# Optimization experiments

Measured on AMD Instinct MI355X. Metric: run time of the kernel, lower is better.

## Reference

```python
import jax, jax.numpy as jnp
import numpy as np

N_NODES = 200000
N_EDGES = 3200000
N_GRAPHS = 1024
NUM_FEATURES = 8


def _glorot(key, shape):
    fan_in, fan_out = shape
    limit = np.sqrt(6.0 / (fan_in + fan_out))
    return jax.random.uniform(key, shape, jnp.float32, -limit, limit)


def setup_inputs() -> dict:
    key = jax.random.key(0)
    ks = jax.random.split(key, 12)
    x = jax.random.normal(ks[0], (N_NODES, NUM_FEATURES), jnp.float32)
    edge_index = jax.random.randint(ks[1], (2, N_EDGES), 0, N_NODES, jnp.int64)
    batch_index = jnp.sort(jax.random.randint(ks[2], (N_NODES,), 0, N_GRAPHS, jnp.int64))
    params = {
        'W0': _glorot(ks[3], (NUM_FEATURES, 64)), 'b0': jnp.zeros((64,), jnp.float32),
        'W1': _glorot(ks[4], (64, 64)),          'b1': jnp.zeros((64,), jnp.float32),
        'W2': _glorot(ks[5], (64, 32)),          'b2': jnp.zeros((32,), jnp.float32),
        'W3': _glorot(ks[6], (32, 32)),          'b3': jnp.zeros((32,), jnp.float32),
        'Wout': _glorot(ks[7], (64, 10)),        'bout': jnp.zeros((10,), jnp.float32),
    }
    return {'x': x, 'edge_index': edge_index, 'batch_index': batch_index, **params}


def _gcn_conv(x, W, b, src, dst, n_nodes):
    """PyG GCNConv: add self-loops, symmetric deg^-1/2 normalization, x@W, scatter-add, +bias."""
    h = x @ W  # [N, out]
    loops = jnp.arange(n_nodes, dtype=src.dtype)
    s = jnp.concatenate([src, loops])
    d = jnp.concatenate([dst, loops])
    ones = jnp.ones_like(d, dtype=h.dtype)
    deg = jax.ops.segment_sum(ones, d, num_segments=n_nodes)  # in-degree incl. self-loop
    dinv = jnp.where(deg > 0, jax.lax.rsqrt(deg), 0.0)
    norm = dinv[s] * dinv[d]  # [E+N]
    msg = h[s] * norm[:, None]  # gather + scale
    agg = jax.ops.segment_sum(msg, d, num_segments=n_nodes)  # scatter-add at target
    return agg + b


def reference(x, edge_index, batch_index, W0, b0, W1, b1, W2, b2, W3, b3, Wout, bout):
    src, dst = edge_index[0], edge_index[1]
    n = x.shape[0]
    h = jnp.tanh(_gcn_conv(x, W0, b0, src, dst, n))
    h = jax.nn.relu(_gcn_conv(h, W1, b1, src, dst, n))
    h = jax.nn.relu(_gcn_conv(h, W2, b2, src, dst, n))
    h = jax.nn.relu(_gcn_conv(h, W3, b3, src, dst, n))
    # global max pool + global mean pool over graphs in the batch
    gmax = jax.ops.segment_max(h, batch_index, num_segments=N_GRAPHS)
    gsum = jax.ops.segment_sum(h, batch_index, num_segments=N_GRAPHS)
    cnt = jax.ops.segment_sum(jnp.ones((n,), h.dtype), batch_index, num_segments=N_GRAPHS)
    gmean = gsum / jnp.maximum(cnt, 1.0)[:, None]
    pooled = jnp.concatenate([gmax, gmean], axis=1)  # [G, 64]
    return pooled @ Wout + bout  # [G, 10]
```

## Files before the change

### kernel.cpp

```cpp
#include <hip/hip_runtime.h>
#include <hip/hip_fp16.h>

#define TPB 256
#define NB_PART 512
#define NB_LOOP 2048

union H8 { float4 f4; __half2 h2[4]; };
union U2H4 { uint2 u2; __half2 h2[2]; };

__device__ inline void acc_h8(const float4& raw, float* a) {
    H8 u; u.f4 = raw;
#pragma unroll
    for (int i = 0; i < 4; i++) {
        float2 f = __half22float2(u.h2[i]);
        a[2 * i] += f.x;
        a[2 * i + 1] += f.y;
    }
}

__device__ inline void acc_h8x2(const float4& rA, const float4& rB, float* a) {
    H8 uA, uB; uA.f4 = rA; uB.f4 = rB;
#pragma unroll
    for (int i = 0; i < 4; i++) {
        float2 fA = __half22float2(uA.h2[i]);
        float2 fB = __half22float2(uB.h2[i]);
        a[2 * i] += fA.x + fB.x;
        a[2 * i + 1] += fA.y + fB.y;
    }
}

__device__ inline void acc_h8p(const float4& rA, const float4& rB, float* a) {
    H8 uA, uB; uA.f4 = rA; uB.f4 = rB;
#pragma unroll
    for (int i = 0; i < 4; i++) {
        __half2 s = __hadd2(uA.h2[i], uB.h2[i]);
        float2 f = __half22float2(s);
        a[2 * i] += f.x;
        a[2 * i + 1] += f.y;
    }
}

__global__ __launch_bounds__(TPB) void k_bhist(const int* __restrict__ dst,
                                               int* __restrict__ bhist, int E, int shift) {
    __shared__ int h[256];
    int tid = threadIdx.x;
    for (int i = tid; i < 256; i += TPB) h[i] = 0;
    __syncthreads();
    int stride = gridDim.x * TPB;
    for (int e = blockIdx.x * TPB + tid; e < E; e += stride)
        atomicAdd(&h[dst[e] >> shift], 1);
    __syncthreads();
    for (int i = tid; i < 256; i += TPB)
        if (h[i]) atomicAdd(&bhist[i], h[i]);
}

__global__ void k_bscan(const int* __restrict__ bhist, int* __restrict__ bstart,
                        int* __restrict__ gcursor, int nbuck) {
    __shared__ int s[256];
    int tid = threadIdx.x;
    int v = bhist[tid];
    s[tid] = v;
    __syncthreads();
    for (int off = 1; off < 256; off <<= 1) {
        int t = (tid >= off) ? s[tid - off] : 0;
        __syncthreads();
        s[tid] += t;
        __syncthreads();
    }
    int excl = s[tid] - v;
    bstart[tid] = excl;
    if (tid == 255) bstart[256] = s[255];
    if (tid < nbuck) gcursor[tid] = excl;
}

__global__ __launch_bounds__(TPB) void k_part(const int* __restrict__ src,
                                              const int* __restrict__ dst,
                                              int* __restrict__ gcursor,
                                              unsigned* __restrict__ staging,
                                              int E, int shift) {
    __shared__ int hist[256];
    __shared__ int base[256];
    int tid = threadIdx.x;
    long long per = (E + gridDim.x - 1) / gridDim.x;
    int e0 = (int)((long long)blockIdx.x * per);
    int e1 = (int)min((long long)E, (long long)e0 + per);
    for (int i = tid; i < 256; i += TPB) hist[i] = 0;
    __syncthreads();
    for (int e = e0 + tid; e < e1; e += TPB) {
        int b = dst[e] >> shift;
        atomicAdd(&hist[b], 1);
    }
    __syncthreads();
    for (int i = tid; i < 256; i += TPB) {
        int c = hist[i];
        base[i] = (c > 0) ? atomicAdd(&gcursor[i], c) : 0;
        hist[i] = 0;
    }
    __syncthreads();
    unsigned lmask = (1u << shift) - 1u;
    for (int e = e0 + tid; e < e1; e += TPB) {
        int d = dst[e];
        int b = d >> shift;
        int p = base[b] + atomicAdd(&hist[b], 1);
        staging[p] = (((unsigned)d & lmask) << 18) | (unsigned)src[e];
    }
}

__global__ __launch_bounds__(TPB) void k_deg_bucket(const unsigned* __restrict__ staging,
                                                    const int* __restrict__ bstart,
                                                    int* __restrict__ deg,
                                                    float* __restrict__ dinv,
                                                    int N, int shift) {
    __shared__ int cnt[4096];
    int b = blockIdx.x;
    int tid = threadIdx.x;
    int base = b << shift;
    int nn = min(1 << shift, N - base);
    for (int i = tid; i < nn; i += TPB) cnt[i] = 0;
    __syncthreads();
    int rs = bstart[b], re = bstart[b + 1];
    for (int j = rs + tid; j < re; j += TPB) atomicAdd(&cnt[staging[j] >> 18], 1);
    __syncthreads();
    for (int i = tid; i < nn; i += TPB) {
        int c = cnt[i];
        deg[base + i] = c;
        dinv[base + i] = rsqrtf((float)c + 1.0f);
    }
}

__global__ __launch_bounds__(TPB) void k_scan1(const int* __restrict__ deg,
                                               int* __restrict__ row_start,
                                               int* __restrict__ bsum, int N) {
    __shared__ int s[TPB];
    int tid = threadIdx.x;
    int i = blockIdx.x * TPB + tid;
    int v = (i < N) ? deg[i] : 0;
    s[tid] = v;
    __syncthreads();
    for (int off = 1; off < TPB; off <<= 1) {
        int t = (tid >= off) ? s[tid - off] : 0;
        __syncthreads();
        s[tid] += t;
        __syncthreads();
    }
    if (i < N) row_start[i] = s[tid] - v;
    if (tid == TPB - 1) bsum[blockIdx.x] = s[tid];
}

__global__ void k_scan2(int* __restrict__ bsum, int nb) {
    __shared__ int s[1024];
    int tid = threadIdx.x;
    int v = (tid < nb) ? bsum[tid] : 0;
    s[tid] = v;
    __syncthreads();
    for (int off = 1; off < 1024; off <<= 1) {
        int t = (tid >= off) ? s[tid - off] : 0;
        __syncthreads();
        s[tid] += t;
        __syncthreads();
    }
    if (tid < nb) bsum[tid] = s[tid] - v;
}

__global__ __launch_bounds__(TPB) void k_scan3(int* __restrict__ row_start,
                                               const int* __restrict__ bsum, int N) {
    int i = blockIdx.x * TPB + threadIdx.x;
    if (i < N) row_start[i] += bsum[blockIdx.x];
}

__global__ __launch_bounds__(TPB) void k_scatter2(const unsigned* __restrict__ staging,
                                                  const int* __restrict__ row_start,
                                                  int* __restrict__ csr,
                                                  int N, int E, int shift) {
    __shared__ int curs[4096];
    int b = blockIdx.x;
    int tid = threadIdx.x;
    int base = b << shift;
    int nn = min(1 << shift, N - base);
    for (int i = tid; i < nn; i += TPB) curs[i] = row_start[base + i];
    __syncthreads();
    int rs = row_start[base];
    int re = (base + nn < N) ? row_start[base + nn] : E;
    for (int j = rs + tid; j < re; j += TPB) {
        unsigned rec = staging[j];
        int s = rec & 0x3FFFF;
        int dl = rec >> 18;
        int p = atomicAdd(&curs[dl], 1);
        csr[p] = s;
    }
}

__global__ __launch_bounds__(TPB) void k_xp16(const float* __restrict__ x,
                                              const float* __restrict__ dinv,
                                              __half* __restrict__ xp, int N) {
    int t = blockIdx.x * TPB + threadIdx.x;
    if (t < N * 8) xp[t] = __float2half(dinv[t >> 3] * x[t]);
}

__global__ __launch_bounds__(TPB) void k_l0fused(const int* __restrict__ row_start,
                                                 const int* __restrict__ deg,
                                                 const int* __restrict__ csr,
                                                 const float* __restrict__ dinv,
                                                 const __half* __restrict__ xp,
                                                 const float* __restrict__ W0,
                                                 const float* __restrict__ b0,
                                                 __half* __restrict__ h0p, int N) {
    int t = blockIdx.x * TPB + threadIdx.x;
    int node = t >> 4;
    int ll = t & 15;
    if (node >= N) return;
    int s0 = row_start[node], dn = deg[node];
    const float4* x4 = (const float4*)xp;
    float a[8] = {0, 0, 0, 0, 0, 0, 0, 0};
    for (int j = ll; j < dn; j += 16) acc_h8(x4[csr[s0 + j]], a);
#pragma unroll
    for (int off = 1; off < 16; off <<= 1) {
#pragma unroll
        for (int i = 0; i < 8; i++) a[i] += __shfl_xor(a[i], off, 64);
    }
    float di = dinv[node];
    H8 u; u.f4 = x4[node];
    float row[8];
#pragma unroll
    for (int i = 0; i < 4; i++) {
        float2 f = __half22float2(u.h2[i]);
        row[2 * i] = di * (a[2 * i] + f.x);
        row[2 * i + 1] = di * (a[2 * i + 1] + f.y);
    }
    float o[4];
#pragma unroll
    for (int c = 0; c < 4; c++) {
        int f = ll * 4 + c;
        float acc = b0[f];
#pragma unroll
        for (int k = 0; k < 8; k++) acc += row[k] * W0[k * 64 + f];
        o[c] = di * tanhf(acc);
    }
    U2H4 w;
    w.h2[0] = __floats2half2_rn(o[0], o[1]);
    w.h2[1] = __floats2half2_rn(o[2], o[3]);
    ((uint2*)h0p)[(size_t)node * 16 + ll] = w.u2;
}

__global__ __launch_bounds__(TPB) void k_pullmm64h(const int* __restrict__ row_start,
                                                   const int* __restrict__ deg,
                                                   const int* __restrict__ csr,
                                                   const float* __restrict__ dinv,
                                                   const __half* __restrict__ h0p,
                                                   const float* __restrict__ W1,
                                                   const float* __restrict__ b1,
                                                   float* __restrict__ h1, int N) {
    __shared__ float Ws[64 * 64];
    __shared__ float rows[4][64];
    int tid = threadIdx.x;
    for (int i = tid; i < 64 * 64; i += TPB) Ws[i] = W1[i];
    __syncthreads();
    int grp = tid >> 6, lane = tid & 63;
    int q = lane & 7, eg = lane >> 3;
    const float4* h4 = (const float4*)h0p;
    int n4 = (N + 3) >> 2;
    for (int blk = blockIdx.x; blk < n4; blk += gridDim.x) {
        int node = blk * 4 + grp;
        if (node < N) {
            int s0 = row_start[node], dn = deg[node];
            float a[8] = {0, 0, 0, 0, 0, 0, 0, 0};
            int j = eg;
            for (; j + 8 < dn; j += 16) {
                int sA = csr[s0 + j];
                int sB = csr[s0 + j + 8];
                float4 vA = h4[(size_t)sA * 8 + q];
                float4 vB = h4[(size_t)sB * 8 + q];
                acc_h8p(vA, vB, a);
            }
            if (j < dn) acc_h8(h4[(size_t)csr[s0 + j] * 8 + q], a);
#pragma unroll
            for (int off = 8; off < 64; off <<= 1) {
#pragma unroll
                for (int i = 0; i < 8; i++) a[i] += __shfl_xor(a[i], off, 64);
            }
            if (eg == 0) {
                float di = dinv[node];
                H8 u; u.f4 = h4[(size_t)node * 8 + q];
#pragma unroll
                for (int i = 0; i < 4; i++) {
                    float2 f = __half22float2(u.h2[i]);
                    rows[grp][q * 8 + 2 * i] = di * (a[2 * i] + f.x);
                    rows[grp][q * 8 + 2 * i + 1] = di * (a[2 * i + 1] + f.y);
                }
            }
            float acc = b1[lane];
#pragma unroll 8
            for (int k = 0; k < 64; k++) acc += rows[grp][k] * Ws[k * 64 + lane];
            h1[(size_t)node * 64 + lane] = fmaxf(acc, 0.0f);
        }
    }
}

__global__ __launch_bounds__(TPB) void k_mmdh(const float* __restrict__ h,
                                              const float* __restrict__ dinv,
                                              const float* __restrict__ W,
                                              __half* __restrict__ out, int N) {
    __shared__ float Ws[64 * 32];
    __shared__ float rows[4][128];
    int tid = threadIdx.x;
    for (int i = tid; i < 64 * 32; i += TPB) Ws[i] = W[i];
    __syncthreads();
    int grp = tid >> 6, lane = tid & 63;
    int which = lane >> 5, f = lane & 31;
    int n8 = (N + 7) >> 3;
    for (int blk = blockIdx.x; blk < n8; blk += gridDim.x) {
        int nbase = blk * 8 + grp * 2;
        if (nbase < N) rows[grp][lane] = h[(size_t)nbase * 64 + lane];
        if (nbase + 1 < N) rows[grp][64 + lane] = h[(size_t)(nbase + 1) * 64 + lane];
        int n = nbase + which;
        if (n < N) {
            float a = 0.0f;
#pragma unroll 8
            for (int k = 0; k < 64; k++) a += rows[grp][which * 64 + k] * Ws[k * 32 + f];
            out[(size_t)n * 32 + f] = __float2half(dinv[n] * a);
        }
    }
}

__global__ __launch_bounds__(TPB) void k_pullfinmm32h(const int* __restrict__ row_start,
                                                      const int* __restrict__ deg,
                                                      const int* __restrict__ csr,
                                                      const float* __restrict__ dinv,
                                                      const __half* __restrict__ t2p,
                                                      const float* __restrict__ b2,
                                                      const float* __restrict__ W3,
                                                      __half* __restrict__ t3p, int N) {
    __shared__ float Ws[32 * 32];
    __shared__ float rows[4][2][32];
    int tid = threadIdx.x;
    for (int i = tid; i < 32 * 32; i += TPB) Ws[i] = W3[i];
    __syncthreads();
    int grp = tid >> 6, lane = tid & 63;
    int hw = lane >> 5, ll = lane & 31;
    int q = ll & 3, eg = ll >> 2;
    const float4* h4 = (const float4*)t2p;
    int n8 = (N + 7) >> 3;
    for (int blk = blockIdx.x; blk < n8; blk += gridDim.x) {
        int node = blk * 8 + grp * 2 + hw;
        if (node < N) {
            float di = dinv[node];
            int s0 = row_start[node], dn = deg[node];
            float a[8] = {0, 0, 0, 0, 0, 0, 0, 0};
            int j = eg;
            for (; j + 8 < dn; j += 16) {
                int sA = csr[s0 + j];
                int sB = csr[s0 + j + 8];
                float4 vA = h4[(size_t)sA * 4 + q];
                float4 vB = h4[(size_t)sB * 4 + q];
                acc_h8x2(vA, vB, a);
            }
            if (j < dn) acc_h8(h4[(size_t)csr[s0 + j] * 4 + q], a);
#pragma unroll
            for (int off = 4; off < 32; off <<= 1) {
#pragma unroll
                for (int i = 0; i < 8; i++) a[i] += __shfl_xor(a[i], off, 64);
            }
            if (eg == 0) {
                H8 u; u.f4 = h4[(size_t)node * 4 + q];
#pragma unroll
                for (int i = 0; i < 4; i++) {
                    float2 f = __half22float2(u.h2[i]);
                    rows[grp][hw][q * 8 + 2 * i] =
                        fmaxf(di * (a[2 * i] + f.x) + b2[q * 8 + 2 * i], 0.0f);
                    rows[grp][hw][q * 8 + 2 * i + 1] =
                        fmaxf(di * (a[2 * i + 1] + f.y) + b2[q * 8 + 2 * i + 1], 0.0f);
                }
            }
            float a2 = 0.0f;
#pragma unroll 8
            for (int k = 0; k < 32; k++) a2 += rows[grp][hw][k] * Ws[k * 32 + ll];
            t3p[(size_t)node * 32 + ll] = __float2half(di * a2);
        }
    }
}

__global__ __launch_bounds__(TPB) void k_pullfin3h(const int* __restrict__ row_start,
                                                   const int* __restrict__ deg,
                                                   const int* __restrict__ csr,
                                                   const float* __restrict__ dinv,
                                                   const __half* __restrict__ t3p,
                                                   const float* __restrict__ b3,
                                                   float* __restrict__ h3, int N) {
    int t = blockIdx.x * TPB + threadIdx.x;
    int node = t >> 5;
    int ll = t & 31;
    if (node >= N) return;
    int q = ll & 3, eg = ll >> 2;
    int s0 = row_start[node], dn = deg[node];
    const float4* h4 = (const float4*)t3p;
    float a[8] = {0, 0, 0, 0, 0, 0, 0, 0};
    int j = eg;
    for (; j + 8 < dn; j += 16) {
        int sA = csr[s0 + j];
        int sB = csr[s0 + j + 8];
        float4 vA = h4[(size_t)sA * 4 + q];
        float4 vB = h4[(size_t)sB * 4 + q];
        acc_h8x2(vA, vB, a);
    }
    if (j < dn) acc_h8(h4[(size_t)csr[s0 + j] * 4 + q], a);
#pragma unroll
    for (int off = 4; off < 32; off <<= 1) {
#pragma unroll
        for (int i = 0; i < 8; i++) a[i] += __shfl_xor(a[i], off, 64);
    }
    if (eg == 0) {
        float di = dinv[node];
        H8 u; u.f4 = h4[(size_t)node * 4 + q];
        float r[8];
#pragma unroll
        for (int i = 0; i < 4; i++) {
            float2 f = __half22float2(u.h2[i]);
            r[2 * i] = fmaxf(di * (a[2 * i] + f.x) + b3[q * 8 + 2 * i], 0.0f);
            r[2 * i + 1] = fmaxf(di * (a[2 * i + 1] + f.y) + b3[q * 8 + 2 * i + 1], 0.0f);
        }
        float4* o = (float4*)h3 + (size_t)node * 8 + q * 2;
        o[0] = make_float4(r[0], r[1], r[2], r[3]);
        o[1] = make_float4(r[4], r[5], r[6], r[7]);
    }
}

__global__ __launch_bounds__(TPB) void k_gbound(const int* __restrict__ batch,
                                                int* __restrict__ start, int N, int G) {
    int g = blockIdx.x * TPB + threadIdx.x;
    if (g > G) return;
    int lo = 0, hi = N;
    while (lo < hi) {
        int mid = (lo + hi) >> 1;
        if (batch[mid] < g) lo = mid + 1;
        else hi = mid;
    }
    start[g] = lo;
}

__global__ __launch_bounds__(TPB) void k_pool2(const float* __restrict__ h,
                                               const int* __restrict__ start,
                                               float* __restrict__ gmax,
                                               float* __restrict__ gsum, int G) {
    __shared__ float smax[8][32];
    __shared__ float ssum[8][32];
    int g = blockIdx.x;
    int s = start[g], e = start[g + 1];
    int tid = threadIdx.x;
    int nl = tid >> 5, f = tid & 31;
    float mx = 0.0f, sm = 0.0f;
    for (int n = s + nl; n < e; n += 8) {
        float v = h[(size_t)n * 32 + f];
        mx = fmaxf(mx, v);
        sm += v;
    }
    smax[nl][f] = mx;
    ssum[nl][f] = sm;
    __syncthreads();
    if (nl == 0) {
#pragma unroll
        for (int k = 1; k < 8; k++) {
            mx = fmaxf(mx, smax[k][f]);
            sm += ssum[k][f];
        }
        gmax[g * 32 + f] = mx;
        gsum[g * 32 + f] = sm;
    }
}

__global__ __launch_bounds__(TPB) void k_out(const float* __restrict__ gmax,
                                             const float* __restrict__ gsum,
                                             const int* __restrict__ start,
                                             const float* __restrict__ Wout,
                                             const float* __restrict__ bout,
                                             float* __restrict__ out, int G) {
    int t = blockIdx.x * TPB + threadIdx.x;
    if (t >= G * 10) return;
    int g = t / 10, j = t % 10;
    float c = (float)(start[g + 1] - start[g]);
    float inv = 1.0f / fmaxf(c, 1.0f);
    float a = bout[j];
#pragma unroll
    for (int k = 0; k < 32; k++) a += gmax[g * 32 + k] * Wout[k * 10 + j];
#pragma unroll
    for (int k = 0; k < 32; k++) a += (gsum[g * 32 + k] * inv) * Wout[(32 + k) * 10 + j];
    out[t] = a;
}

static inline int cdiv(long long a, int b) { return (int)((a + b - 1) / b); }

extern "C" void kernel_launch(void* const* d_in, const int* in_sizes, int n_in,
                              void* d_out, int out_size, void* d_ws, size_t ws_size,
                              hipStream_t stream) {
    const float* x    = (const float*)d_in[0];
    const int*   ei   = (const int*)d_in[1];
    const int*   bidx = (const int*)d_in[2];
    const float* W0 = (const float*)d_in[3];
    const float* b0 = (const float*)d_in[4];
    const float* W1 = (const float*)d_in[5];
    const float* b1 = (const float*)d_in[6];
    const float* W2 = (const float*)d_in[7];
    const float* b2 = (const float*)d_in[8];
    const float* W3 = (const float*)d_in[9];
    const float* b3 = (const float*)d_in[10];
    const float* Wout = (const float*)d_in[11];
    const float* bout = (const float*)d_in[12];
    float* out = (float*)d_out;

    const int N = in_sizes[0] / 8;
    const int E = in_sizes[1] / 2;
    const int G = out_size / 10;
    const int* src = ei;
    const int* dst = ei + E;

    int shift = 10;
    while (((N + (1 << shift) - 1) >> shift) > 256) shift++;
    const int nbuck = (N + (1 << shift) - 1) >> shift;

    char* w = (char*)d_ws;
    int*   deg_i     = (int*)w;    w += (size_t)N * 4;
    int*   row_start = (int*)w;    w += (size_t)N * 4;
    float* dinv      = (float*)w;  w += (size_t)N * 4;
    float* gmax      = (float*)w;  w += (size_t)G * 32 * 4;
    float* gsum      = (float*)w;  w += (size_t)G * 32 * 4;
    int*   gstart    = (int*)w;    w += (size_t)(G + 4) * 4;
    int*   bhist     = (int*)w;    w += 256 * 4;
    int*   bstart    = (int*)w;    w += 260 * 4;
    int*   csr       = (int*)w;    w += (size_t)E * 4;
    float* bufA      = (float*)w;  w += (size_t)N * 64 * 4;
    float* bufB      = (float*)w;  w += (size_t)N * 64 * 4;
    unsigned* staging = (unsigned*)bufA;
    int*      bsum    = (int*)bufB;
    int*      gcursor = (int*)bufB + 1024;
    __half* xp16  = (__half*)bufB;
    __half* h0p16 = (__half*)bufA;
    float*  h1    = (float*)bufB;
    __half* t2p16 = (__half*)bufA;
    __half* t3p16 = (__half*)bufB;
    float*  h3    = (float*)bufA;

    const int nb = cdiv(N, TPB);

    hipMemsetAsync(bhist, 0, 256 * 4, stream);
    k_bhist<<<256, TPB, 0, stream>>>(dst, bhist, E, shift);
    k_bscan<<<1, 256, 0, stream>>>(bhist, bstart, gcursor, nbuck);
    k_part<<<NB_PART, TPB, 0, stream>>>(src, dst, gcursor, staging, E, shift);
    k_deg_bucket<<<nbuck, TPB, 0, stream>>>(staging, bstart, deg_i, dinv, N, shift);
    k_scan1<<<nb, TPB, 0, stream>>>(deg_i, row_start, bsum, N);
    k_scan2<<<1, 1024, 0, stream>>>(bsum, nb);
    k_scan3<<<nb, TPB, 0, stream>>>(row_start, bsum, N);
    k_scatter2<<<nbuck, TPB, 0, stream>>>(staging, row_start, csr, N, E, shift);
    k_gbound<<<cdiv(G + 1, TPB), TPB, 0, stream>>>(bidx, gstart, N, G);

    k_xp16<<<cdiv((long long)N * 8, TPB), TPB, 0, stream>>>(x, dinv, xp16, N);
    k_l0fused<<<cdiv(N, 16), TPB, 0, stream>>>(row_start, deg_i, csr, dinv, xp16, W0, b0,
                                               h0p16, N);

    k_pullmm64h<<<NB_LOOP, TPB, 0, stream>>>(row_start, deg_i, csr, dinv, h0p16, W1, b1,
                                             h1, N);

    k_mmdh<<<NB_LOOP, TPB, 0, stream>>>(h1, dinv, W2, t2p16, N);
    k_pullfinmm32h<<<NB_LOOP, TPB, 0, stream>>>(row_start, deg_i, csr, dinv, t2p16, b2,
                                                W3, t3p16, N);

    k_pullfin3h<<<cdiv(N, 8), TPB, 0, stream>>>(row_start, deg_i, csr, dinv, t3p16, b3, h3, N);

    k_pool2<<<G, TPB, 0, stream>>>(h3, gstart, gmax, gsum, G);
    k_out<<<cdiv((long long)G * 10, TPB), TPB, 0, stream>>>(gmax, gsum, gstart, Wout, bout,
                                                            out, G);
}
```

Baseline: 700.8 us.

## Fuse degree count with row-start scan and fuse layer-1 pull with W2 matmul

Degree counting and the exclusive scan for CSR row starts now happen in one per-bucket kernel, using the bucket start offset as the base, so three scan kernels go away. The layer-1 pull-aggregate plus W1 matmul is fused with the following W2 projection, which removes the fp32 h1 round trip through global memory. Each wave now processes two nodes with interleaved edge loops to raise memory-level parallelism. In exchange the fused kernel uses more shared memory and registers, and nodes of unequal degree can leave lanes idle in the interleaved loop.

```diff
diff --git a/kernel.cpp b/kernel.cpp
--- a/kernel.cpp
+++ b/kernel.cpp
@@ -106,14 +106,15 @@
     }
 }
 
-__global__ __launch_bounds__(TPB) void k_deg_bucket(const unsigned* __restrict__ staging,
-                                                    const int* __restrict__ bstart,
-                                                    int* __restrict__ deg,
-                                                    float* __restrict__ dinv,
-                                                    int N, int shift) {
+__global__ __launch_bounds__(TPB) void k_deg_scan(const unsigned* __restrict__ staging,
+                                                  const int* __restrict__ bstart,
+                                                  int* __restrict__ deg,
+                                                  float* __restrict__ dinv,
+                                                  int* __restrict__ row_start,
+                                                  int N, int shift) {
     __shared__ int cnt[4096];
-    int b = blockIdx.x;
-    int tid = threadIdx.x;
+    __shared__ int sums[TPB];
+    int b = blockIdx.x, tid = threadIdx.x;
     int base = b << shift;
     int nn = min(1 << shift, N - base);
     for (int i = tid; i < nn; i += TPB) cnt[i] = 0;
@@ -121,51 +122,32 @@
     int rs = bstart[b], re = bstart[b + 1];
     for (int j = rs + tid; j < re; j += TPB) atomicAdd(&cnt[staging[j] >> 18], 1);
     __syncthreads();
-    for (int i = tid; i < nn; i += TPB) {
-        int c = cnt[i];
-        deg[base + i] = c;
-        dinv[base + i] = rsqrtf((float)c + 1.0f);
-    }
-}
-
-__global__ __launch_bounds__(TPB) void k_scan1(const int* __restrict__ deg,
-                                               int* __restrict__ row_start,
-                                               int* __restrict__ bsum, int N) {
-    __shared__ int s[TPB];
-    int tid = threadIdx.x;
-    int i = blockIdx.x * TPB + tid;
-    int v = (i < N) ? deg[i] : 0;
-    s[tid] = v;
+    int per = (nn + TPB - 1) / TPB;
+    int myb = tid * per;
+    int loc = 0;
+    for (int c = 0; c < per; c++) {
+        int idx = myb + c;
+        if (idx < nn) loc += cnt[idx];
+    }
+    sums[tid] = loc;
     __syncthreads();
     for (int off = 1; off < TPB; off <<= 1) {
-        int t = (tid >= off) ? s[tid - off] : 0;
+        int t = (tid >= off) ? sums[tid - off] : 0;
         __syncthreads();
-        s[tid] += t;
+        sums[tid] += t;
         __syncthreads();
     }
-    if (i < N) row_start[i] = s[tid] - v;
-    if (tid == TPB - 1) bsum[blockIdx.x] = s[tid];
-}
-
-__global__ void k_scan2(int* __restrict__ bsum, int nb) {
-    __shared__ int s[1024];
-    int tid = threadIdx.x;
-    int v = (tid < nb) ? bsum[tid] : 0;
-    s[tid] = v;
-    __syncthreads();
-    for (int off = 1; off < 1024; off <<= 1) {
-        int t = (tid >= off) ? s[tid - off] : 0;
-        __syncthreads();
-        s[tid] += t;
-        __syncthreads();
-    }
-    if (tid < nb) bsum[tid] = s[tid] - v;
-}
-
-__global__ __launch_bounds__(TPB) void k_scan3(int* __restrict__ row_start,
-                                               const int* __restrict__ bsum, int N) {
-    int i = blockIdx.x * TPB + threadIdx.x;
-    if (i < N) row_start[i] += bsum[blockIdx.x];
+    int running = rs + sums[tid] - loc;
+    for (int c = 0; c < per; c++) {
+        int idx = myb + c;
+        if (idx < nn) {
+            int v = cnt[idx];
+            deg[base + idx] = v;
+            dinv[base + idx] = rsqrtf((float)v + 1.0f);
+            row_start[base + idx] = running;
+            running += v;
+        }
+    }
 }
 
 __global__ __launch_bounds__(TPB) void k_scatter2(const unsigned* __restrict__ staging,
@@ -242,82 +224,101 @@
     ((uint2*)h0p)[(size_t)node * 16 + ll] = w.u2;
 }
 
-__global__ __launch_bounds__(TPB) void k_pullmm64h(const int* __restrict__ row_start,
-                                                   const int* __restrict__ deg,
-                                                   const int* __restrict__ csr,
-                                                   const float* __restrict__ dinv,
-                                                   const __half* __restrict__ h0p,
-                                                   const float* __restrict__ W1,
-                                                   const float* __restrict__ b1,
-                                                   float* __restrict__ h1, int N) {
-    __shared__ float Ws[64 * 64];
+__global__ __launch_bounds__(TPB) void k_pullmmf(const int* __restrict__ row_start,
+                                                 const int* __restrict__ deg,
+                                                 const int* __restrict__ csr,
+                                                 const float* __restrict__ dinv,
+                                                 const __half* __restrict__ h0p,
+                                                 const float* __restrict__ W1,
+                                                 const float* __restrict__ b1,
+                                                 const float* __restrict__ W2,
+                                                 __half* __restrict__ t2p, int N) {
+    __shared__ float W1s[64 * 64];
+    __shared__ float W2s[64 * 32];
     __shared__ float rows[4][64];
-    int tid = threadIdx.x;
-    for (int i = tid; i < 64 * 64; i += TPB) Ws[i] = W1[i];
+    __shared__ float h1s[4][64];
+    int tid = threadIdx.x;
+    for (int i = tid; i < 64 * 64; i += TPB) W1s[i] = W1[i];
+    for (int i = tid; i < 64 * 32; i += TPB) W2s[i] = W2[i];
     __syncthreads();
     int grp = tid >> 6, lane = tid & 63;
     int q = lane & 7, eg = lane >> 3;
+    int hf = lane >> 5, f = lane & 31;
     const float4* h4 = (const float4*)h0p;
-    int n4 = (N + 3) >> 2;
-    for (int blk = blockIdx.x; blk < n4; blk += gridDim.x) {
-        int node = blk * 4 + grp;
-        if (node < N) {
-            int s0 = row_start[node], dn = deg[node];
-            float a[8] = {0, 0, 0, 0, 0, 0, 0, 0};
-            int j = eg;
-            for (; j + 8 < dn; j += 16) {
-                int sA = csr[s0 + j];
-                int sB = csr[s0 + j + 8];
-                float4 vA = h4[(size_t)sA * 8 + q];
-                float4 vB = h4[(size_t)sB * 8 + q];
-                acc_h8p(vA, vB, a);
+    int n8 = (N + 7) >> 3;
+    for (int blk = blockIdx.x; blk < n8; blk += gridDim.x) {
+        int nA = blk * 8 + grp * 2;
+        int nB = nA + 1;
+        if (nA >= N) continue;
+        bool hasB = nB < N;
+        int2 rs2 = *(const int2*)(row_start + nA);
+        int2 dg2 = *(const int2*)(deg + nA);
+        int s0A = rs2.x, dnA = dg2.x;
+        int s0B = rs2.y, dnB = hasB ? dg2.y : 0;
+        float aA[8] = {0, 0, 0, 0, 0, 0, 0, 0};
+        float aB[8] = {0, 0, 0, 0, 0, 0, 0, 0};
+        int jA = eg, jB = eg;
+        while ((jA + 8 < dnA) || (jB + 8 < dnB)) {
+            bool mA = jA + 8 < dnA, mB = jB + 8 < dnB;
+            int sA0 = 0, sA1 = 0, sB0 = 0, sB1 = 0;
+            if (mA) { sA0 = csr[s0A + jA]; sA1 = csr[s0A + jA + 8]; }
+            if (mB) { sB0 = csr[s0B + jB]; sB1 = csr[s0B + jB + 8]; }
+            float4 vA0, vA1, vB0, vB1;
+            if (mA) { vA0 = h4[(size_t)sA0 * 8 + q]; vA1 = h4[(size_t)sA1 * 8 + q]; }
+            if (mB) { vB0 = h4[(size_t)sB0 * 8 + q]; vB1 = h4[(size_t)sB1 * 8 + q]; }
+            if (mA) { acc_h8p(vA0, vA1, aA); jA += 16; }
+            if (mB) { acc_h8p(vB0, vB1, aB); jB += 16; }
+        }
+        if (jA < dnA) acc_h8(h4[(size_t)csr[s0A + jA] * 8 + q], aA);
+        if (jB < dnB) acc_h8(h4[(size_t)csr[s0B + jB] * 8 + q], aB);
+#pragma unroll
+        for (int off = 8; off < 64; off <<= 1) {
+#pragma unroll
+            for (int i = 0; i < 8; i++) {
+                aA[i] += __shfl_xor(aA[i], off, 64);
+                aB[i] += __shfl_xor(aB[i], off, 64);
             }
-            if (j < dn) acc_h8(h4[(size_t)csr[s0 + j] * 8 + q], a);
-#pragma unroll
-            for (int off = 8; off < 64; off <<= 1) {
-#pragma unroll
-                for (int i = 0; i < 8; i++) a[i] += __shfl_xor(a[i], off, 64);
+        }
+        float diA = dinv[nA];
+        if (eg == 0) {
+            H8 u; u.f4 = h4[(size_t)nA * 8 + q];
+#pragma unroll
+            for (int i = 0; i < 4; i++) {
+                float2 fv = __half22float2(u.h2[i]);
+                rows[grp][q * 8 + 2 * i] = diA * (aA[2 * i] + fv.x);
+                rows[grp][q * 8 + 2 * i + 1] = diA * (aA[2 * i + 1] + fv.y);
             }
+        }
+        float acc = b1[lane];
+#pragma unroll 8
+        for (int k = 0; k < 64; k++) acc += rows[grp][k] * W1s[k * 64 + lane];
+        h1s[grp][lane] = fmaxf(acc, 0.0f);
+        float p = 0.0f;
+#pragma unroll 8
+        for (int k = 0; k < 32; k++) p += h1s[grp][hf * 32 + k] * W2s[(hf * 32 + k) * 32 + f];
+        p += __shfl_xor(p, 32, 64);
+        if (hf == 0) t2p[(size_t)nA * 32 + f] = __float2half(diA * p);
+        if (hasB) {
+            float diB = dinv[nB];
             if (eg == 0) {
-                float di = dinv[node];
-                H8 u; u.f4 = h4[(size_t)node * 8 + q];
+                H8 u; u.f4 = h4[(size_t)nB * 8 + q];
 #pragma unroll
                 for (int i = 0; i < 4; i++) {
-                    float2 f = __half22float2(u.h2[i]);
-                    rows[grp][q * 8 + 2 * i] = di * (a[2 * i] + f.x);
-                    rows[grp][q * 8 + 2 * i + 1] = di * (a[2 * i + 1] + f.y);
+                    float2 fv = __half22float2(u.h2[i]);
+                    rows[grp][q * 8 + 2 * i] = diB * (aB[2 * i] + fv.x);
+                    rows[grp][q * 8 + 2 * i + 1] = diB * (aB[2 * i + 1] + fv.y);
                 }
             }
-            float acc = b1[lane];
+            float accB = b1[lane];
 #pragma unroll 8
-            for (int k = 0; k < 64; k++) acc += rows[grp][k] * Ws[k * 64 + lane];
-            h1[(size_t)node * 64 + lane] = fmaxf(acc, 0.0f);
-        }
-    }
-}
-
-__global__ __launch_bounds__(TPB) void k_mmdh(const float* __restrict__ h,
-                                              const float* __restrict__ dinv,
-                                              const float* __restrict__ W,
-                                              __half* __restrict__ out, int N) {
-    __shared__ float Ws[64 * 32];
-    __shared__ float rows[4][128];
-    int tid = threadIdx.x;
-    for (int i = tid; i < 64 * 32; i += TPB) Ws[i] = W[i];
-    __syncthreads();
-    int grp = tid >> 6, lane = tid & 63;
-    int which = lane >> 5, f = lane & 31;
-    int n8 = (N + 7) >> 3;
-    for (int blk = blockIdx.x; blk < n8; blk += gridDim.x) {
-        int nbase = blk * 8 + grp * 2;
-        if (nbase < N) rows[grp][lane] = h[(size_t)nbase * 64 + lane];
-        if (nbase + 1 < N) rows[grp][64 + lane] = h[(size_t)(nbase + 1) * 64 + lane];
-        int n = nbase + which;
-        if (n < N) {
-            float a = 0.0f;
+            for (int k = 0; k < 64; k++) accB += rows[grp][k] * W1s[k * 64 + lane];
+            h1s[grp][lane] = fmaxf(accB, 0.0f);
+            float pB = 0.0f;
 #pragma unroll 8
-            for (int k = 0; k < 64; k++) a += rows[grp][which * 64 + k] * Ws[k * 32 + f];
-            out[(size_t)n * 32 + f] = __float2half(dinv[n] * a);
+            for (int k = 0; k < 32; k++)
+                pB += h1s[grp][hf * 32 + k] * W2s[(hf * 32 + k) * 32 + f];
+            pB += __shfl_xor(pB, 32, 64);
+            if (hf == 0) t2p[(size_t)nB * 32 + f] = __float2half(diB * pB);
         }
     }
 }
@@ -529,25 +530,18 @@
     float* bufA      = (float*)w;  w += (size_t)N * 64 * 4;
     float* bufB      = (float*)w;  w += (size_t)N * 64 * 4;
     unsigned* staging = (unsigned*)bufA;
-    int*      bsum    = (int*)bufB;
-    int*      gcursor = (int*)bufB + 1024;
+    int*      gcursor = (int*)bufB;
     __half* xp16  = (__half*)bufB;
     __half* h0p16 = (__half*)bufA;
-    float*  h1    = (float*)bufB;
-    __half* t2p16 = (__half*)bufA;
-    __half* t3p16 = (__half*)bufB;
-    float*  h3    = (float*)bufA;
-
-    const int nb = cdiv(N, TPB);
+    __half* t2p16 = (__half*)bufB;
+    __half* t3p16 = (__half*)bufA;
+    float*  h3    = (float*)bufB;
 
     hipMemsetAsync(bhist, 0, 256 * 4, stream);
     k_bhist<<<256, TPB, 0, stream>>>(dst, bhist, E, shift);
     k_bscan<<<1, 256, 0, stream>>>(bhist, bstart, gcursor, nbuck);
     k_part<<<NB_PART, TPB, 0, stream>>>(src, dst, gcursor, staging, E, shift);
-    k_deg_bucket<<<nbuck, TPB, 0, stream>>>(staging, bstart, deg_i, dinv, N, shift);
-    k_scan1<<<nb, TPB, 0, stream>>>(deg_i, row_start, bsum, N);
-    k_scan2<<<1, 1024, 0, stream>>>(bsum, nb);
-    k_scan3<<<nb, TPB, 0, stream>>>(row_start, bsum, N);
+    k_deg_scan<<<nbuck, TPB, 0, stream>>>(staging, bstart, deg_i, dinv, row_start, N, shift);
     k_scatter2<<<nbuck, TPB, 0, stream>>>(staging, row_start, csr, N, E, shift);
     k_gbound<<<cdiv(G + 1, TPB), TPB, 0, stream>>>(bidx, gstart, N, G);
 
@@ -555,10 +549,9 @@
     k_l0fused<<<cdiv(N, 16), TPB, 0, stream>>>(row_start, deg_i, csr, dinv, xp16, W0, b0,
                                                h0p16, N);
 
-    k_pullmm64h<<<NB_LOOP, TPB, 0, stream>>>(row_start, deg_i, csr, dinv, h0p16, W1, b1,
-                                             h1, N);
-
-    k_mmdh<<<NB_LOOP, TPB, 0, stream>>>(h1, dinv, W2, t2p16, N);
+    k_pullmmf<<<NB_LOOP, TPB, 0, stream>>>(row_start, deg_i, csr, dinv, h0p16, W1, b1, W2,
+                                           t2p16, N);
+
     k_pullfinmm32h<<<NB_LOOP, TPB, 0, stream>>>(row_start, deg_i, csr, dinv, t2p16, b2,
                                                 W3, t3p16, N);
 
```

Result: no change. 689.7 us (-1.6%).

## Fuse degree count with row-start scan and fuse last pull with pooling

Applied to the files above, without the earlier changes.

Computes the CSR row_start prefix directly inside the per-bucket degree kernel using the bucket start offset, removing three separate scan kernels. Also merges the final-layer aggregation with global max/mean pooling by processing each graph's nodes in one block, so the h3 intermediate never goes to memory. The fused pull-pool kernel launches one block per graph, reducing available parallelism for the latency-bound gather.

```diff
diff --git a/kernel.cpp b/kernel.cpp
--- a/kernel.cpp
+++ b/kernel.cpp
@@ -106,14 +106,15 @@
     }
 }
 
-__global__ __launch_bounds__(TPB) void k_deg_bucket(const unsigned* __restrict__ staging,
-                                                    const int* __restrict__ bstart,
-                                                    int* __restrict__ deg,
-                                                    float* __restrict__ dinv,
-                                                    int N, int shift) {
+__global__ __launch_bounds__(TPB) void k_deg_scan(const unsigned* __restrict__ staging,
+                                                  const int* __restrict__ bstart,
+                                                  int* __restrict__ deg,
+                                                  float* __restrict__ dinv,
+                                                  int* __restrict__ row_start,
+                                                  int N, int shift) {
     __shared__ int cnt[4096];
-    int b = blockIdx.x;
-    int tid = threadIdx.x;
+    __shared__ int sums[TPB];
+    int b = blockIdx.x, tid = threadIdx.x;
     int base = b << shift;
     int nn = min(1 << shift, N - base);
     for (int i = tid; i < nn; i += TPB) cnt[i] = 0;
@@ -121,51 +122,32 @@
     int rs = bstart[b], re = bstart[b + 1];
     for (int j = rs + tid; j < re; j += TPB) atomicAdd(&cnt[staging[j] >> 18], 1);
     __syncthreads();
-    for (int i = tid; i < nn; i += TPB) {
-        int c = cnt[i];
-        deg[base + i] = c;
-        dinv[base + i] = rsqrtf((float)c + 1.0f);
-    }
-}
-
-__global__ __launch_bounds__(TPB) void k_scan1(const int* __restrict__ deg,
-                                               int* __restrict__ row_start,
-                                               int* __restrict__ bsum, int N) {
-    __shared__ int s[TPB];
-    int tid = threadIdx.x;
-    int i = blockIdx.x * TPB + tid;
-    int v = (i < N) ? deg[i] : 0;
-    s[tid] = v;
+    int per = (nn + TPB - 1) / TPB;
+    int myb = tid * per;
+    int loc = 0;
+    for (int c = 0; c < per; c++) {
+        int idx = myb + c;
+        if (idx < nn) loc += cnt[idx];
+    }
+    sums[tid] = loc;
     __syncthreads();
     for (int off = 1; off < TPB; off <<= 1) {
-        int t = (tid >= off) ? s[tid - off] : 0;
+        int t = (tid >= off) ? sums[tid - off] : 0;
         __syncthreads();
-        s[tid] += t;
+        sums[tid] += t;
         __syncthreads();
     }
-    if (i < N) row_start[i] = s[tid] - v;
-    if (tid == TPB - 1) bsum[blockIdx.x] = s[tid];
-}
-
-__global__ void k_scan2(int* __restrict__ bsum, int nb) {
-    __shared__ int s[1024];
-    int tid = threadIdx.x;
-    int v = (tid < nb) ? bsum[tid] : 0;
-    s[tid] = v;
-    __syncthreads();
-    for (int off = 1; off < 1024; off <<= 1) {
-        int t = (tid >= off) ? s[tid - off] : 0;
-        __syncthreads();
-        s[tid] += t;
-        __syncthreads();
-    }
-    if (tid < nb) bsum[tid] = s[tid] - v;
-}
-
-__global__ __launch_bounds__(TPB) void k_scan3(int* __restrict__ row_start,
-                                               const int* __restrict__ bsum, int N) {
-    int i = blockIdx.x * TPB + threadIdx.x;
-    if (i < N) row_start[i] += bsum[blockIdx.x];
+    int running = rs + sums[tid] - loc;
+    for (int c = 0; c < per; c++) {
+        int idx = myb + c;
+        if (idx < nn) {
+            int v = cnt[idx];
+            deg[base + idx] = v;
+            dinv[base + idx] = rsqrtf((float)v + 1.0f);
+            row_start[base + idx] = running;
+            running += v;
+        }
+    }
 }
 
 __global__ __launch_bounds__(TPB) void k_scatter2(const unsigned* __restrict__ staging,
@@ -379,48 +361,76 @@
     }
 }
 
-__global__ __launch_bounds__(TPB) void k_pullfin3h(const int* __restrict__ row_start,
-                                                   const int* __restrict__ deg,
-                                                   const int* __restrict__ csr,
-                                                   const float* __restrict__ dinv,
-                                                   const __half* __restrict__ t3p,
-                                                   const float* __restrict__ b3,
-                                                   float* __restrict__ h3, int N) {
-    int t = blockIdx.x * TPB + threadIdx.x;
-    int node = t >> 5;
-    int ll = t & 31;
-    if (node >= N) return;
+__global__ __launch_bounds__(TPB) void k_pullpool(const int* __restrict__ row_start,
+                                                  const int* __restrict__ deg,
+                                                  const int* __restrict__ csr,
+                                                  const float* __restrict__ dinv,
+                                                  const __half* __restrict__ t3p,
+                                                  const float* __restrict__ b3,
+                                                  const int* __restrict__ gstart,
+                                                  float* __restrict__ gmax,
+                                                  float* __restrict__ gsum, int G) {
+    __shared__ float smax[8][32];
+    __shared__ float ssum[8][32];
+    int g = blockIdx.x;
+    int s = gstart[g], e = gstart[g + 1];
+    int tid = threadIdx.x;
+    int wv = tid >> 6, lane = tid & 63;
+    int hw = lane >> 5, ll = lane & 31;
     int q = ll & 3, eg = ll >> 2;
-    int s0 = row_start[node], dn = deg[node];
+    int slot = wv * 2 + hw;
     const float4* h4 = (const float4*)t3p;
-    float a[8] = {0, 0, 0, 0, 0, 0, 0, 0};
-    int j = eg;
-    for (; j + 8 < dn; j += 16) {
-        int sA = csr[s0 + j];
-        int sB = csr[s0 + j + 8];
-        float4 vA = h4[(size_t)sA * 4 + q];
-        float4 vB = h4[(size_t)sB * 4 + q];
-        acc_h8x2(vA, vB, a);
-    }
-    if (j < dn) acc_h8(h4[(size_t)csr[s0 + j] * 4 + q], a);
-#pragma unroll
-    for (int off = 4; off < 32; off <<= 1) {
-#pragma unroll
-        for (int i = 0; i < 8; i++) a[i] += __shfl_xor(a[i], off, 64);
+    float mx[8] = {0, 0, 0, 0, 0, 0, 0, 0};
+    float sm[8] = {0, 0, 0, 0, 0, 0, 0, 0};
+    for (int node = s + slot; node < e; node += 8) {
+        int s0 = row_start[node], dn = deg[node];
+        float a[8] = {0, 0, 0, 0, 0, 0, 0, 0};
+        int j = eg;
+        for (; j + 8 < dn; j += 16) {
+            int sA = csr[s0 + j];
+            int sB = csr[s0 + j + 8];
+            float4 vA = h4[(size_t)sA * 4 + q];
+            float4 vB = h4[(size_t)sB * 4 + q];
+            acc_h8x2(vA, vB, a);
+        }
+        if (j < dn) acc_h8(h4[(size_t)csr[s0 + j] * 4 + q], a);
+#pragma unroll
+        for (int off = 4; off < 32; off <<= 1) {
+#pragma unroll
+            for (int i = 0; i < 8; i++) a[i] += __shfl_xor(a[i], off, 64);
+        }
+        if (eg == 0) {
+            float di = dinv[node];
+            H8 u; u.f4 = h4[(size_t)node * 4 + q];
+#pragma unroll
+            for (int i = 0; i < 4; i++) {
+                float2 f = __half22float2(u.h2[i]);
+                float r0 = fmaxf(di * (a[2 * i] + f.x) + b3[q * 8 + 2 * i], 0.0f);
+                float r1 = fmaxf(di * (a[2 * i + 1] + f.y) + b3[q * 8 + 2 * i + 1], 0.0f);
+                mx[2 * i] = fmaxf(mx[2 * i], r0);
+                mx[2 * i + 1] = fmaxf(mx[2 * i + 1], r1);
+                sm[2 * i] += r0;
+                sm[2 * i + 1] += r1;
+            }
+        }
     }
     if (eg == 0) {
-        float di = dinv[node];
-        H8 u; u.f4 = h4[(size_t)node * 4 + q];
-        float r[8];
-#pragma unroll
-        for (int i = 0; i < 4; i++) {
-            float2 f = __half22float2(u.h2[i]);
-            r[2 * i] = fmaxf(di * (a[2 * i] + f.x) + b3[q * 8 + 2 * i], 0.0f);
-            r[2 * i + 1] = fmaxf(di * (a[2 * i + 1] + f.y) + b3[q * 8 + 2 * i + 1], 0.0f);
-        }
-        float4* o = (float4*)h3 + (size_t)node * 8 + q * 2;
-        o[0] = make_float4(r[0], r[1], r[2], r[3]);
-        o[1] = make_float4(r[4], r[5], r[6], r[7]);
+#pragma unroll
+        for (int i = 0; i < 8; i++) {
+            smax[slot][q * 8 + i] = mx[i];
+            ssum[slot][q * 8 + i] = sm[i];
+        }
+    }
+    __syncthreads();
+    if (tid < 32) {
+        float M = 0.0f, S = 0.0f;
+#pragma unroll
+        for (int k = 0; k < 8; k++) {
+            M = fmaxf(M, smax[k][tid]);
+            S += ssum[k][tid];
+        }
+        gmax[g * 32 + tid] = M;
+        gsum[g * 32 + tid] = S;
     }
 }
 
@@ -435,36 +445,6 @@
         else hi = mid;
     }
     start[g] = lo;
-}
-
-__global__ __launch_bounds__(TPB) void k_pool2(const float* __restrict__ h,
-                                               const int* __restrict__ start,
-                                               float* __restrict__ gmax,
-                                               float* __restrict__ gsum, int G) {
-    __shared__ float smax[8][32];
-    __shared__ float ssum[8][32];
-    int g = blockIdx.x;
-    int s = start[g], e = start[g + 1];
-    int tid = threadIdx.x;
-    int nl = tid >> 5, f = tid & 31;
-    float mx = 0.0f, sm = 0.0f;
-    for (int n = s + nl; n < e; n += 8) {
-        float v = h[(size_t)n * 32 + f];
-        mx = fmaxf(mx, v);
-        sm += v;
-    }
-    smax[nl][f] = mx;
-    ssum[nl][f] = sm;
-    __syncthreads();
-    if (nl == 0) {
-#pragma unroll
-        for (int k = 1; k < 8; k++) {
-            mx = fmaxf(mx, smax[k][f]);
-            sm += ssum[k][f];
-        }
-        gmax[g * 32 + f] = mx;
-        gsum[g * 32 + f] = sm;
-    }
 }
 
 __global__ __launch_bounds__(TPB) void k_out(const float* __restrict__ gmax,
@@ -529,25 +509,18 @@
     float* bufA      = (float*)w;  w += (size_t)N * 64 * 4;
     float* bufB      = (float*)w;  w += (size_t)N * 64 * 4;
     unsigned* staging = (unsigned*)bufA;
-    int*      bsum    = (int*)bufB;
-    int*      gcursor = (int*)bufB + 1024;
+    int*      gcursor = (int*)bufB;
     __half* xp16  = (__half*)bufB;
     __half* h0p16 = (__half*)bufA;
     float*  h1    = (float*)bufB;
     __half* t2p16 = (__half*)bufA;
     __half* t3p16 = (__half*)bufB;
-    float*  h3    = (float*)bufA;
-
-    const int nb = cdiv(N, TPB);
 
     hipMemsetAsync(bhist, 0, 256 * 4, stream);
     k_bhist<<<256, TPB, 0, stream>>>(dst, bhist, E, shift);
     k_bscan<<<1, 256, 0, stream>>>(bhist, bstart, gcursor, nbuck);
     k_part<<<NB_PART, TPB, 0, stream>>>(src, dst, gcursor, staging, E, shift);
-    k_deg_bucket<<<nbuck, TPB, 0, stream>>>(staging, bstart, deg_i, dinv, N, shift);
-    k_scan1<<<nb, TPB, 0, stream>>>(deg_i, row_start, bsum, N);
-    k_scan2<<<1, 1024, 0, stream>>>(bsum, nb);
-    k_scan3<<<nb, TPB, 0, stream>>>(row_start, bsum, N);
+    k_deg_scan<<<nbuck, TPB, 0, stream>>>(staging, bstart, deg_i, dinv, row_start, N, shift);
     k_scatter2<<<nbuck, TPB, 0, stream>>>(staging, row_start, csr, N, E, shift);
     k_gbound<<<cdiv(G + 1, TPB), TPB, 0, stream>>>(bidx, gstart, N, G);
 
@@ -562,9 +535,9 @@
     k_pullfinmm32h<<<NB_LOOP, TPB, 0, stream>>>(row_start, deg_i, csr, dinv, t2p16, b2,
                                                 W3, t3p16, N);
 
-    k_pullfin3h<<<cdiv(N, 8), TPB, 0, stream>>>(row_start, deg_i, csr, dinv, t3p16, b3, h3, N);
-
-    k_pool2<<<G, TPB, 0, stream>>>(h3, gstart, gmax, gsum, G);
+    k_pullpool<<<G, TPB, 0, stream>>>(row_start, deg_i, csr, dinv, t3p16, b3, gstart,
+                                      gmax, gsum, G);
+
     k_out<<<cdiv((long long)G * 10, TPB), TPB, 0, stream>>>(gmax, gsum, gstart, Wout, bout,
                                                             out, G);
 }
```

New measurement: 694.8 us. Within noise of the previous version (-0.9%).
